# Kernel optimization log

Hardware: AMD Instinct MI355X
Metric: run time of the kernel (lower is better)

## Reference

```python
import jax, jax.numpy as jnp
import numpy as np


def setup_inputs() -> dict:
    key = jax.random.key(0)
    k1, k2, k3, k4 = jax.random.split(key, 4)
    B, T, C, H = 8, 2048, 1024, 64
    x = jax.random.normal(k1, (B, T, C), dtype=jnp.float32)
    Wq = jax.random.normal(k2, (C, H), dtype=jnp.float32) * (C ** -0.5)
    Wk = jax.random.normal(k3, (C, H), dtype=jnp.float32) * (C ** -0.5)
    Wv = jax.random.normal(k4, (C, H), dtype=jnp.float32) * (C ** -0.5)
    return {"x": x, "Wq": Wq, "Wk": Wk, "Wv": Wv}


def reference(x, Wq, Wk, Wv):
    # x: [B,T,C]; Wq/Wk/Wv: [C,H] (nn.Linear bias=False => x @ W)
    B, T, C = x.shape
    H = Wq.shape[-1]
    q = jnp.einsum('btc,ch->bth', x, Wq)
    k = jnp.einsum('btc,ch->bth', x, Wk)
    v = jnp.einsum('btc,ch->bth', x, Wv)
    scale = H ** -0.5
    att = jnp.einsum('bqh,bkh->bqk', q, k) * scale  # [B,T,T]
    causal = jnp.tril(jnp.ones((T, T), dtype=bool))
    att = jnp.where(causal, att, -jnp.inf)
    att = jax.nn.softmax(att, axis=-1)
    out = jnp.einsum('bqk,bkh->bqh', att, v)  # [B,T,H]
    return out
```

## Files before the change

### kernel.cpp

```cpp
#include <hip/hip_runtime.h>
#include <hip/hip_bf16.h>
#include <math.h>

#define BB 8
#define TT 2048
#define CC 1024
#define HH 64
#define BT (BB * TT)

typedef __attribute__((ext_vector_type(8))) short short8;
typedef __attribute__((ext_vector_type(4))) float floatx4;

static __device__ inline ushort f2bf(float f) {
    __hip_bfloat16 h = __float2bfloat16(f);
    return *reinterpret_cast<ushort*>(&h);
}
static __device__ inline unsigned int f2bf2(float lo, float hi) {
    __hip_bfloat162 h = __float22bfloat162_rn(make_float2(lo, hi));
    return *reinterpret_cast<unsigned int*>(&h);
}
static __device__ inline float bf2f(ushort u) {
    union { unsigned int i; float f; } c;
    c.i = ((unsigned int)u) << 16;
    return c.f;
}

__global__ __launch_bounds__(256) void wprep_kernel(
    const float* __restrict__ Wq, const float* __restrict__ Wk,
    const float* __restrict__ Wv, ushort* __restrict__ WbT)
{
    __shared__ float ws_[64 * 65];
    const int m  = blockIdx.x >> 4;
    const int kb = (blockIdx.x & 15) * 64;
    const float* W = (m == 0) ? Wq : (m == 1) ? Wk : Wv;
    const int t  = threadIdx.x;
    const int lr = t >> 4, lc = (t & 15) * 4;
    #pragma unroll
    for (int i = 0; i < 4; ++i) {
        const int row = lr + i * 16;
        float4 v = *(const float4*)&W[(size_t)(kb + row) * HH + lc];
        ws_[row * 65 + lc + 0] = v.x; ws_[row * 65 + lc + 1] = v.y;
        ws_[row * 65 + lc + 2] = v.z; ws_[row * 65 + lc + 3] = v.w;
    }
    __syncthreads();
    const int n = t & 63, kseg = t >> 6;
    union { ushort s[16]; uint4 q[2]; } u;
    #pragma unroll
    for (int j = 0; j < 16; ++j)
        u.s[j] = f2bf(ws_[(kseg * 16 + j) * 65 + n]);
    ushort* dst = &WbT[(size_t)(m * 64 + n) * 1024 + kb + kseg * 16];
    *(uint4*)&dst[0] = u.q[0];
    *(uint4*)&dst[8] = u.q[1];
}

__global__ __launch_bounds__(256) void qkv_kernel(
    const float* __restrict__ x, const ushort* __restrict__ WbT,
    ushort* __restrict__ qb, ushort* __restrict__ kbS, ushort* __restrict__ vS)
{
    __shared__ __align__(16) ushort As[2][1024];

    const int row0 = blockIdx.x * 16;
    const int t    = threadIdx.x;
    const int w    = t >> 6;
    const int lane = t & 63;
    const int l16  = lane & 15;
    const int quad = lane >> 4;
    const int ct0  = w * 3;

    const int srow = t >> 4, sseg = t & 15;
    const int sp = sseg >> 3, squad = (sseg >> 1) & 3, shalf = sseg & 1;
    const int widx = (((sp * 64 + srow * 4 + squad) * 8) + shalf * 4)
                     ^ ((srow & 7) << 3);
    const float* xsrc = &x[(size_t)(row0 + srow) * CC + sseg * 4];

    const int ridx0 = ((l16 * 4 + quad) * 8)       ^ ((l16 & 7) << 3);
    const int ridx1 = ((64 + l16 * 4 + quad) * 8)  ^ ((l16 & 7) << 3);

    floatx4 acc[3];
    #pragma unroll
    for (int c = 0; c < 3; ++c) acc[c] = (floatx4){0.f, 0.f, 0.f, 0.f};

    float4 xc = *(const float4*)&xsrc[0];
    float4 xn;

    short8 bfr[2][3], bnx[2][3];
    #pragma unroll
    for (int p = 0; p < 2; ++p)
        #pragma unroll
        for (int c = 0; c < 3; ++c)
            bfr[p][c] = *(const short8*)&WbT[(size_t)((ct0 + c) * 16 + l16) * 1024
                                             + p * 32 + quad * 8];

    for (int it = 0; it < 16; ++it) {
        uint2 uq;
        uq.x = f2bf2(xc.x, xc.y);
        uq.y = f2bf2(xc.z, xc.w);
        *(uint2*)&As[it & 1][widx] = uq;
        __syncthreads();

        if (it < 15) {
            xn = *(const float4*)&xsrc[(it + 1) * 64];
            const int kn = (it + 1) * 64;
            #pragma unroll
            for (int p = 0; p < 2; ++p)
                #pragma unroll
                for (int c = 0; c < 3; ++c)
                    bnx[p][c] = *(const short8*)&WbT[(size_t)((ct0 + c) * 16 + l16) * 1024
                                                     + kn + p * 32 + quad * 8];
        }

        short8 a0 = *(const short8*)&As[it & 1][ridx0];
        short8 a1 = *(const short8*)&As[it & 1][ridx1];

        __builtin_amdgcn_s_setprio(1);
        #pragma unroll
        for (int c = 0; c < 3; ++c) {
            acc[c] = __builtin_amdgcn_mfma_f32_16x16x32_bf16(a0, bfr[0][c], acc[c], 0, 0, 0);
            acc[c] = __builtin_amdgcn_mfma_f32_16x16x32_bf16(a1, bfr[1][c], acc[c], 0, 0, 0);
        }
        __builtin_amdgcn_s_setprio(0);

        xc = xn;
        #pragma unroll
        for (int p = 0; p < 2; ++p)
            #pragma unroll
            for (int c = 0; c < 3; ++c) bfr[p][c] = bnx[p][c];
    }

    const int half = (row0 >> 5) & 1;
    const int mt   = (row0 >> 4) & 1;
    const size_t tile = (size_t)(row0 >> 6) * 4096;
    #pragma unroll
    for (int c = 0; c < 3; ++c) {
        const int ct    = ct0 + c;
        const int mtype = ct >> 2;
        const int n0    = (ct & 3) * 16;
        const int row   = row0 + quad * 4;
        if (mtype == 0) {
            #pragma unroll
            for (int reg = 0; reg < 4; ++reg)
                qb[(size_t)(row + reg) * HH + n0 + l16] = f2bf(acc[c][reg] * 0.125f);
        } else if (mtype == 1) {
            const int cP    = half * 2 + mt;
            const int pP    = (ct & 3) >> 1;
            const int quadP = ((ct & 3) * 2 + (l16 >> 3)) & 3;
            const int jP    = l16 & 7;
            const int ub    = (cP * 2 + pP) * 64 + quadP * 16;
            #pragma unroll
            for (int reg = 0; reg < 4; ++reg)
                kbS[tile + (size_t)(ub + quad * 4 + reg) * 8 + jP] = f2bf(acc[c][reg]);
        } else {
            const int cp2 = (ct & 3) * 2 + half;
            #pragma unroll
            for (int reg = 0; reg < 4; ++reg) {
                const int rq    = quad * 4 + reg;
                const int quadP = mt * 2 + (rq >> 3);
                vS[tile + (size_t)(cp2 * 64 + quadP * 16 + l16) * 8 + (rq & 7)] = f2bf(acc[c][reg]);
            }
        }
    }
}

__global__ __launch_bounds__(256) void attn_kernel(
    const ushort* __restrict__ qb, const ushort* __restrict__ kbS,
    const ushort* __restrict__ vS, ushort* __restrict__ Opart,
    float* __restrict__ ml)
{
    __shared__ __align__(16) ushort P[4][16 * 72];

    const int t    = threadIdx.x;
    const int w    = t >> 6;
    const int lane = t & 63;
    const int l16  = lane & 15;
    const int quad = lane >> 4;

    const int b   = blockIdx.x & 7;
    const int idx = blockIdx.x >> 3;
    int qt, part, np;
    if (idx < 32)      { qt = 31 - (idx >> 2); part = idx & 3; np = 4; }
    else if (idx < 56) { const int u = idx - 32; const int g = u / 3;
                         qt = 23 - g; part = u - g * 3; np = 3; }
    else if (idx < 72) { const int u = idx - 56; qt = 15 - (u >> 1); part = u & 1; np = 2; }
    else               { qt = 7 - (idx - 72); part = 0; np = 1; }
    const int ntiles = qt + 1;
    const int ktb = (part * ntiles) / np;
    const int kte = ((part + 1) * ntiles) / np;

    const ushort* ktile0 = kbS + (size_t)(b * 32) * 4096;
    const ushort* vtile0 = vS  + (size_t)(b * 32) * 4096;

    short8 qf[2];
    {
        const ushort* qrow = qb + ((size_t)b * TT + qt * 64 + w * 16) * HH;
        qf[0] = *(const short8*)&qrow[l16 * HH + quad * 8];
        qf[1] = *(const short8*)&qrow[l16 * HH + 32 + quad * 8];
    }
    short8 ones;
    #pragma unroll
    for (int i = 0; i < 8; ++i) ones[i] = (short)0x3F80;

    floatx4 o[4], osum;
    #pragma unroll
    for (int c = 0; c < 4; ++c) o[c] = (floatx4){0.f, 0.f, 0.f, 0.f};
    osum = (floatx4){0.f, 0.f, 0.f, 0.f};

    ushort* Pw = &P[w][0];

    for (int kt = ktb; kt < kte; ++kt) {
        const ushort* kg = ktile0 + (size_t)kt * 4096;
        const ushort* vg = vtile0 + (size_t)kt * 4096;

        short8 kf[4][2];
        #pragma unroll
        for (int c = 0; c < 4; ++c)
            #pragma unroll
            for (int p = 0; p < 2; ++p)
                kf[c][p] = *(const short8*)&kg[(size_t)(((c * 2 + p) * 64) + lane) * 8];

        floatx4 s[4];
        #pragma unroll
        for (int c = 0; c < 4; ++c) s[c] = (floatx4){0.f, 0.f, 0.f, 0.f};
        __builtin_amdgcn_s_setprio(1);
        #pragma unroll
        for (int c = 0; c < 4; ++c)
            #pragma unroll
            for (int p = 0; p < 2; ++p)
                s[c] = __builtin_amdgcn_mfma_f32_16x16x32_bf16(kf[c][p], qf[p], s[c], 0, 0, 0);
        __builtin_amdgcn_s_setprio(0);

        short8 vf[4][2];
        #pragma unroll
        for (int c = 0; c < 4; ++c)
            #pragma unroll
            for (int p = 0; p < 2; ++p)
                vf[c][p] = *(const short8*)&vg[(size_t)(((c * 2 + p) * 64) + lane) * 8];

        if (kt == ntiles - 1) {
            const int key0 = kt * 64 + quad * 4;
            const int qrow = qt * 64 + w * 16 + l16;
            #pragma unroll
            for (int c = 0; c < 4; ++c)
                #pragma unroll
                for (int reg = 0; reg < 4; ++reg)
                    if (key0 + c * 16 + reg > qrow) s[c][reg] = -1e30f;
        }

        #pragma unroll
        for (int c = 0; c < 4; ++c) {
            uint2 u;
            u.x = f2bf2(__expf(s[c][0]), __expf(s[c][1]));
            u.y = f2bf2(__expf(s[c][2]), __expf(s[c][3]));
            *(uint2*)&Pw[l16 * 72 + c * 16 + quad * 4] = u;
        }

        short8 pf[2];
        pf[0] = *(const short8*)&Pw[l16 * 72 + quad * 8];
        pf[1] = *(const short8*)&Pw[l16 * 72 + 32 + quad * 8];

        __builtin_amdgcn_s_setprio(1);
        #pragma unroll
        for (int p = 0; p < 2; ++p) {
            #pragma unroll
            for (int c = 0; c < 4; ++c)
                o[c] = __builtin_amdgcn_mfma_f32_16x16x32_bf16(pf[p], vf[c][p], o[c], 0, 0, 0);
            osum = __builtin_amdgcn_mfma_f32_16x16x32_bf16(pf[p], ones, osum, 0, 0, 0);
        }
        __builtin_amdgcn_s_setprio(0);
    }

    const size_t ub = (size_t)blockIdx.x * 4096;
    const int rbase = w * 16 + quad * 4;
    #pragma unroll
    for (int c = 0; c < 4; ++c) {
        uint2 u;
        u.x = f2bf2(o[c][0], o[c][1]);
        u.y = f2bf2(o[c][2], o[c][3]);
        *(uint2*)&Opart[ub + (size_t)(c * 16 + l16) * 64 + rbase] = u;
    }
    if (l16 == 0) {
        #pragma unroll
        for (int reg = 0; reg < 4; ++reg)
            ml[(size_t)blockIdx.x * 64 + rbase + reg] = osum[reg];
    }
}

__global__ __launch_bounds__(256) void merge_kernel(
    const ushort* __restrict__ Opart, const float* __restrict__ ml,
    float* __restrict__ out)
{
    const int t    = threadIdx.x;
    const int gw   = blockIdx.x * 4 + (t >> 6);
    const int lane = t & 63;
    const int b    = gw >> 8;
    const int v    = gw & 255;
    const int qt   = v >> 3;
    const int oct  = v & 7;

    int base, np;
    if (qt >= 24)      { base = (31 - qt) * 4;      np = 4; }
    else if (qt >= 16) { base = 32 + (23 - qt) * 3; np = 3; }
    else if (qt >= 8)  { base = 56 + (15 - qt) * 2; np = 2; }
    else               { base = 72 + (7 - qt);      np = 1; }

    float* obase = out + ((size_t)b * TT + qt * 64) * HH;

    #pragma unroll
    for (int rg = 0; rg < 2; ++rg) {
        const int row0 = oct * 8 + rg * 4;
        float dx = 0.f, dy = 0.f, dz = 0.f, dw = 0.f;
        float ax = 0.f, ay = 0.f, az = 0.f, aw = 0.f;
        for (int p = 0; p < np; ++p) {
            const int unit = (base + p) * 8 + b;
            float4 d = *(const float4*)&ml[(size_t)unit * 64 + row0];
            dx += d.x; dy += d.y; dz += d.z; dw += d.w;
            ushort4 ov = *(const ushort4*)&Opart[(size_t)unit * 4096 + lane * 64 + row0];
            ax += bf2f(ov.x); ay += bf2f(ov.y); az += bf2f(ov.z); aw += bf2f(ov.w);
        }
        obase[(size_t)(row0 + 0) * HH + lane] = ax / dx;
        obase[(size_t)(row0 + 1) * HH + lane] = ay / dy;
        obase[(size_t)(row0 + 2) * HH + lane] = az / dz;
        obase[(size_t)(row0 + 3) * HH + lane] = aw / dw;
    }
}

extern "C" void kernel_launch(void* const* d_in, const int* in_sizes, int n_in,
                              void* d_out, int out_size, void* d_ws, size_t ws_size,
                              hipStream_t stream)
{
    (void)in_sizes; (void)n_in; (void)out_size; (void)ws_size;
    const float* x  = (const float*)d_in[0];
    const float* Wq = (const float*)d_in[1];
    const float* Wk = (const float*)d_in[2];
    const float* Wv = (const float*)d_in[3];
    float* outp = (float*)d_out;

    char* base = (char*)d_ws;
    ushort* WbT   = (ushort*)(base);
    ushort* qbuf  = (ushort*)(base + 393216);
    ushort* kbS   = qbuf + (size_t)BT * HH;
    ushort* vSb   = kbS + (size_t)BT * HH;
    ushort* Opart = vSb + (size_t)BT * HH;
    float*  ml    = (float*)((char*)Opart + (size_t)640 * 4096 * 2);

    wprep_kernel<<<dim3(48),   256, 0, stream>>>(Wq, Wk, Wv, WbT);
    qkv_kernel  <<<dim3(1024), 256, 0, stream>>>(x, WbT, qbuf, kbS, vSb);
    attn_kernel <<<dim3(640),  256, 0, stream>>>(qbuf, kbS, vSb, Opart, ml);
    merge_kernel<<<dim3(512),  256, 0, stream>>>(Opart, ml, outp);
}
```

Measured before the change: 154.5 us.

## Restructure QKV projection to load x directly into registers and compute transposed tiles

The QKV projection kernel no longer stages bf16-converted x through shared memory with a barrier per k-step. Each lane now loads its own x fragment straight from global memory into the MFMA B operand, and weights become the A operand, so the output is computed transposed. Each wave covers 16 rows by 6 column tiles, and each block now covers 32 rows, which halves the grid. Loads are double-buffered two steps ahead and the output stores are rewritten to be vectorised for the transposed accumulator layout. In exchange, register pressure rises (launch bounds now target 2 blocks) and x global loads become less coalesced.

```diff
diff --git a/kernel.cpp b/kernel.cpp
--- a/kernel.cpp
+++ b/kernel.cpp
@@ -53,110 +53,113 @@
     *(uint4*)&dst[8] = u.q[1];
 }
 
-__global__ __launch_bounds__(256) void qkv_kernel(
+__global__ __launch_bounds__(256, 2) void qkv_kernel(
     const float* __restrict__ x, const ushort* __restrict__ WbT,
     ushort* __restrict__ qb, ushort* __restrict__ kbS, ushort* __restrict__ vS)
 {
-    __shared__ __align__(16) ushort As[2][1024];
-
-    const int row0 = blockIdx.x * 16;
     const int t    = threadIdx.x;
     const int w    = t >> 6;
     const int lane = t & 63;
     const int l16  = lane & 15;
     const int quad = lane >> 4;
-    const int ct0  = w * 3;
-
-    const int srow = t >> 4, sseg = t & 15;
-    const int sp = sseg >> 3, squad = (sseg >> 1) & 3, shalf = sseg & 1;
-    const int widx = (((sp * 64 + srow * 4 + squad) * 8) + shalf * 4)
-                     ^ ((srow & 7) << 3);
-    const float* xsrc = &x[(size_t)(row0 + srow) * CC + sseg * 4];
-
-    const int ridx0 = ((l16 * 4 + quad) * 8)       ^ ((l16 & 7) << 3);
-    const int ridx1 = ((64 + l16 * 4 + quad) * 8)  ^ ((l16 & 7) << 3);
-
-    floatx4 acc[3];
-    #pragma unroll
-    for (int c = 0; c < 3; ++c) acc[c] = (floatx4){0.f, 0.f, 0.f, 0.f};
-
-    float4 xc = *(const float4*)&xsrc[0];
-    float4 xn;
-
-    short8 bfr[2][3], bnx[2][3];
+
+    const int rows0 = blockIdx.x * 32 + (w >> 1) * 16;
+    const int ct0   = (w & 1) * 6;
+
+    const float* xr = &x[(size_t)(rows0 + l16) * CC + quad * 8];
+    const ushort* wb = &WbT[(size_t)l16 * 1024 + quad * 8];
+
+    floatx4 acc[6];
+    #pragma unroll
+    for (int c = 0; c < 6; ++c) acc[c] = (floatx4){0.f, 0.f, 0.f, 0.f};
+
+    float4 xcA[2][2], xcB[2][2];
+    #pragma unroll
+    for (int p = 0; p < 2; ++p) {
+        xcA[p][0] = *(const float4*)&xr[p * 32 + 0];
+        xcA[p][1] = *(const float4*)&xr[p * 32 + 4];
+        xcB[p][0] = *(const float4*)&xr[64 + p * 32 + 0];
+        xcB[p][1] = *(const float4*)&xr[64 + p * 32 + 4];
+    }
+
+    short8 afA[2][6], afB[2][6];
     #pragma unroll
     for (int p = 0; p < 2; ++p)
         #pragma unroll
-        for (int c = 0; c < 3; ++c)
-            bfr[p][c] = *(const short8*)&WbT[(size_t)((ct0 + c) * 16 + l16) * 1024
-                                             + p * 32 + quad * 8];
-
-    for (int it = 0; it < 16; ++it) {
-        uint2 uq;
-        uq.x = f2bf2(xc.x, xc.y);
-        uq.y = f2bf2(xc.z, xc.w);
-        *(uint2*)&As[it & 1][widx] = uq;
-        __syncthreads();
-
-        if (it < 15) {
-            xn = *(const float4*)&xsrc[(it + 1) * 64];
-            const int kn = (it + 1) * 64;
+        for (int c = 0; c < 6; ++c)
+            afA[p][c] = *(const short8*)&wb[(size_t)(ct0 + c) * 16384 + p * 32];
+
+    auto body = [&](int it, float4 (&xc)[2][2], short8 (&aCur)[2][6], short8 (&aNxt)[2][6]) {
+        short8 bx[2];
+        #pragma unroll
+        for (int p = 0; p < 2; ++p) {
+            union { unsigned int u[4]; short8 s; } cv;
+            cv.u[0] = f2bf2(xc[p][0].x, xc[p][0].y);
+            cv.u[1] = f2bf2(xc[p][0].z, xc[p][0].w);
+            cv.u[2] = f2bf2(xc[p][1].x, xc[p][1].y);
+            cv.u[3] = f2bf2(xc[p][1].z, xc[p][1].w);
+            bx[p] = cv.s;
+        }
+        if (it + 2 < 16) {
+            #pragma unroll
+            for (int p = 0; p < 2; ++p) {
+                xc[p][0] = *(const float4*)&xr[(it + 2) * 64 + p * 32 + 0];
+                xc[p][1] = *(const float4*)&xr[(it + 2) * 64 + p * 32 + 4];
+            }
+        }
+        if (it + 1 < 16) {
             #pragma unroll
             for (int p = 0; p < 2; ++p)
                 #pragma unroll
-                for (int c = 0; c < 3; ++c)
-                    bnx[p][c] = *(const short8*)&WbT[(size_t)((ct0 + c) * 16 + l16) * 1024
-                                                     + kn + p * 32 + quad * 8];
-        }
-
-        short8 a0 = *(const short8*)&As[it & 1][ridx0];
-        short8 a1 = *(const short8*)&As[it & 1][ridx1];
-
+                for (int c = 0; c < 6; ++c)
+                    aNxt[p][c] = *(const short8*)&wb[(size_t)(ct0 + c) * 16384
+                                                     + (it + 1) * 64 + p * 32];
+        }
         __builtin_amdgcn_s_setprio(1);
         #pragma unroll
-        for (int c = 0; c < 3; ++c) {
-            acc[c] = __builtin_amdgcn_mfma_f32_16x16x32_bf16(a0, bfr[0][c], acc[c], 0, 0, 0);
-            acc[c] = __builtin_amdgcn_mfma_f32_16x16x32_bf16(a1, bfr[1][c], acc[c], 0, 0, 0);
-        }
+        for (int p = 0; p < 2; ++p)
+            #pragma unroll
+            for (int c = 0; c < 6; ++c)
+                acc[c] = __builtin_amdgcn_mfma_f32_16x16x32_bf16(aCur[p][c], bx[p], acc[c], 0, 0, 0);
         __builtin_amdgcn_s_setprio(0);
-
-        xc = xn;
-        #pragma unroll
-        for (int p = 0; p < 2; ++p)
-            #pragma unroll
-            for (int c = 0; c < 3; ++c) bfr[p][c] = bnx[p][c];
-    }
-
-    const int half = (row0 >> 5) & 1;
-    const int mt   = (row0 >> 4) & 1;
-    const size_t tile = (size_t)(row0 >> 6) * 4096;
-    #pragma unroll
-    for (int c = 0; c < 3; ++c) {
+    };
+
+    #pragma unroll 1
+    for (int it2 = 0; it2 < 16; it2 += 4) {
+        body(it2 + 0, xcA, afA, afB);
+        body(it2 + 1, xcB, afB, afA);
+        body(it2 + 2, xcA, afA, afB);
+        body(it2 + 3, xcB, afB, afA);
+    }
+
+    const size_t tile = (size_t)(rows0 >> 6) * 4096;
+    #pragma unroll
+    for (int c = 0; c < 6; ++c) {
         const int ct    = ct0 + c;
         const int mtype = ct >> 2;
-        const int n0    = (ct & 3) * 16;
-        const int row   = row0 + quad * 4;
+        const int nn    = ct & 3;
         if (mtype == 0) {
+            uint2 u;
+            u.x = f2bf2(acc[c][0] * 0.125f, acc[c][1] * 0.125f);
+            u.y = f2bf2(acc[c][2] * 0.125f, acc[c][3] * 0.125f);
+            *(uint2*)&qb[(size_t)(rows0 + l16) * HH + nn * 16 + quad * 4] = u;
+        } else if (mtype == 1) {
+            const int ckey  = (rows0 >> 4) & 3;
+            const int p     = nn >> 1;
+            const int quadP = (nn * 2 + (quad >> 1)) & 3;
+            const int j0    = (quad & 1) * 4;
+            uint2 u;
+            u.x = f2bf2(acc[c][0], acc[c][1]);
+            u.y = f2bf2(acc[c][2], acc[c][3]);
+            *(uint2*)&kbS[tile + (size_t)((ckey * 2 + p) * 64 + quadP * 16 + l16) * 8 + j0] = u;
+        } else {
+            const int pv = (rows0 >> 5) & 1;
+            const int qv = ((rows0 >> 4) & 1) * 2 + (l16 >> 3);
+            const int jv = l16 & 7;
             #pragma unroll
             for (int reg = 0; reg < 4; ++reg)
-                qb[(size_t)(row + reg) * HH + n0 + l16] = f2bf(acc[c][reg] * 0.125f);
-        } else if (mtype == 1) {
-            const int cP    = half * 2 + mt;
-            const int pP    = (ct & 3) >> 1;
-            const int quadP = ((ct & 3) * 2 + (l16 >> 3)) & 3;
-            const int jP    = l16 & 7;
-            const int ub    = (cP * 2 + pP) * 64 + quadP * 16;
-            #pragma unroll
-            for (int reg = 0; reg < 4; ++reg)
-                kbS[tile + (size_t)(ub + quad * 4 + reg) * 8 + jP] = f2bf(acc[c][reg]);
-        } else {
-            const int cp2 = (ct & 3) * 2 + half;
-            #pragma unroll
-            for (int reg = 0; reg < 4; ++reg) {
-                const int rq    = quad * 4 + reg;
-                const int quadP = mt * 2 + (rq >> 3);
-                vS[tile + (size_t)(cp2 * 64 + quadP * 16 + l16) * 8 + (rq & 7)] = f2bf(acc[c][reg]);
-            }
+                vS[tile + (size_t)((nn * 2 + pv) * 64 + qv * 16 + quad * 4 + reg) * 8 + jv]
+                    = f2bf(acc[c][reg]);
         }
     }
 }
@@ -342,8 +345,8 @@
     ushort* Opart = vSb + (size_t)BT * HH;
     float*  ml    = (float*)((char*)Opart + (size_t)640 * 4096 * 2);
 
-    wprep_kernel<<<dim3(48),   256, 0, stream>>>(Wq, Wk, Wv, WbT);
-    qkv_kernel  <<<dim3(1024), 256, 0, stream>>>(x, WbT, qbuf, kbS, vSb);
-    attn_kernel <<<dim3(640),  256, 0, stream>>>(qbuf, kbS, vSb, Opart, ml);
-    merge_kernel<<<dim3(512),  256, 0, stream>>>(Opart, ml, outp);
-}
+    wprep_kernel<<<dim3(48),  256, 0, stream>>>(Wq, Wk, Wv, WbT);
+    qkv_kernel  <<<dim3(512), 256, 0, stream>>>(x, WbT, qbuf, kbS, vSb);
+    attn_kernel <<<dim3(640), 256, 0, stream>>>(qbuf, kbS, vSb, Opart, ml);
+    merge_kernel<<<dim3(512), 256, 0, stream>>>(Opart, ml, outp);
+}
```

After: 165.2 us. 6.9% more time.
